# Performance work log

Measured on AMD Instinct MI355X. Metric: run time of the kernel, lower is better.

Reference implementation:

```python
import jax, jax.numpy as jnp
import numpy as np

K = 3  # knnLoss default k


def _knn_loss(source_pc, target_pc, k=K):
    """Faithful translation of knnLoss.forward.

    For each batch: drop exact-zero (0,0,0) points from both clouds
    (emulated via masking for static shapes), find the k nearest *target*
    points for every *source* point (query=source, ref=target), take the
    mean Euclidean distance, then average over batch.
    """

    def per_batch(src, tgt):  # src, tgt: [N, 3]
        src_valid = jnp.any(src != 0.0, axis=-1)  # [Ns] move_zero_point mask
        tgt_valid = jnp.any(tgt != 0.0, axis=-1)  # [Nt]
        s2 = jnp.sum(src * src, axis=-1)          # [Ns]
        t2 = jnp.sum(tgt * tgt, axis=-1)          # [Nt]
        # squared pairwise distances, [Ns, Nt]
        d2 = s2[:, None] + t2[None, :] - 2.0 * (src @ tgt.T)
        d2 = jnp.maximum(d2, 0.0)
        # invalid (zero) target points can never be a neighbor
        d2 = jnp.where(tgt_valid[None, :], d2, jnp.inf)
        neg_top, _ = jax.lax.top_k(-d2, k)        # k smallest squared dists
        dist = jnp.sqrt(-neg_top)                 # [Ns, k] euclidean, like KNN_CUDA
        # mean over valid source points x k neighbors
        num = jnp.sum(jnp.where(src_valid[:, None], dist, 0.0))
        den = jnp.sum(src_valid).astype(dist.dtype) * k
        return num / den

    return jnp.mean(jax.vmap(per_batch)(source_pc, target_pc))


def setup_inputs() -> dict:
    key = jax.random.key(0)
    k1, k2 = jax.random.split(key)
    B, N = 4, 8192
    source_pc = jax.random.normal(k1, (B, N, 3), dtype=jnp.float32)
    target_pc = jax.random.normal(k2, (B, N, 3), dtype=jnp.float32)
    return {"source_pc": source_pc, "target_pc": target_pc}


def reference(source_pc, target_pc):
    return _knn_loss(source_pc, target_pc)
```

## Files before the change

kernel.cpp:

```cpp
#include <hip/hip_runtime.h>
#include <math.h>

#define BATCH 4
#define NPTS 8192
#define TILE 512
#define TSPLIT 16
#define SRC_PER_BLOCK 512
#define SRC_CHUNKS 16
#define NSRC_TOT (BATCH * NPTS)

typedef __attribute__((ext_vector_type(2))) float f2;
typedef __attribute__((ext_vector_type(4))) float f4;

__device__ __forceinline__ f2 pk_fma(f2 a, f2 b, f2 c) {
    f2 d;
    asm("v_pk_fma_f32 %0, %1, %2, %3" : "=v"(d) : "v"(a), "v"(b), "v"(c));
    return d;
}

__device__ __forceinline__ void insert3(float d, float& a0, float& a1, float& a2) {
    float h = fmaxf(a1, d);
    float m = __builtin_amdgcn_fmed3f(a0, a1, d);
    a2 = fminf(a2, h);
    a1 = m;
    a0 = fminf(a0, d);
}

__device__ __forceinline__ void merge33(float a0, float a1, float a2,
                                        float& b0, float& b1, float& b2) {
    float s0 = fminf(a0, b0);
    float h  = fmaxf(a0, b0);
    float m  = fminf(a1, b1);
    float mm = fminf(a2, b2);
    b1 = fminf(h, m);
    b2 = __builtin_amdgcn_fmed3f(h, m, mm);
    b0 = s0;
}

__global__ __launch_bounds__(256) void knn_partial(const float* __restrict__ src,
                                                   const float* __restrict__ tgt,
                                                   float* __restrict__ part,
                                                   float* __restrict__ hdr) {
    __shared__ f4 ts[TILE / 2 * 2];
    const int tid = threadIdx.x;
    const int sc = blockIdx.x, tc = blockIdx.y, b = blockIdx.z;

    if (sc == 0 && tc == 0 && b == 0 && tid < 16) hdr[tid] = 0.0f;

    {
        const float* tb = tgt + ((size_t)b * NPTS + (size_t)tc * TILE + 2 * tid) * 3;
        float x0 = tb[0], y0 = tb[1], z0 = tb[2];
        float x1 = tb[3], y1 = tb[4], z1 = tb[5];
        float w0 = 0.5f * (x0 * x0 + y0 * y0 + z0 * z0);
        float w1 = 0.5f * (x1 * x1 + y1 * y1 + z1 * z1);
        if (!(x0 != 0.f || y0 != 0.f || z0 != 0.f)) w0 = 1.0e38f;
        if (!(x1 != 0.f || y1 != 0.f || z1 != 0.f)) w1 = 1.0e38f;
        ts[2 * tid + 0] = (f4){x0, x1, y0, y1};
        ts[2 * tid + 1] = (f4){z0, z1, w0, w1};
    }
    __syncthreads();

    f2 nx[2], ny[2], nz[2];
    #pragma unroll
    for (int s = 0; s < 2; ++s) {
        int i = sc * SRC_PER_BLOCK + tid + 256 * s;
        const float* sp = src + ((size_t)b * NPTS + i) * 3;
        float ax = sp[0], ay = sp[1], az = sp[2];
        nx[s] = (f2){-ax, -ax};
        ny[s] = (f2){-ay, -ay};
        nz[s] = (f2){-az, -az};
    }

    float c0[2][2], c1[2][2], c2[2][2];
    #pragma unroll
    for (int s = 0; s < 2; ++s)
        for (int h = 0; h < 2; ++h) { c0[s][h] = c1[s][h] = c2[s][h] = 3e38f; }

    #pragma unroll 8
    for (int e = 0; e < TILE / 2; ++e) {
        f4 p = ts[2 * e + 0];
        f4 q = ts[2 * e + 1];
        f2 xs = __builtin_shufflevector(p, p, 0, 1);
        f2 ys = __builtin_shufflevector(p, p, 2, 3);
        f2 zs = __builtin_shufflevector(q, q, 0, 1);
        f2 wh = __builtin_shufflevector(q, q, 2, 3);
        #pragma unroll
        for (int s = 0; s < 2; ++s) {
            f2 v = pk_fma(xs, nx[s], wh);
            v = pk_fma(ys, ny[s], v);
            v = pk_fma(zs, nz[s], v);
            insert3(v.x, c0[s][0], c1[s][0], c2[s][0]);
            insert3(v.y, c0[s][1], c1[s][1], c2[s][1]);
        }
    }

    #pragma unroll
    for (int s = 0; s < 2; ++s) {
        merge33(c0[s][1], c1[s][1], c2[s][1], c0[s][0], c1[s][0], c2[s][0]);
        size_t flat = (size_t)b * NPTS + sc * SRC_PER_BLOCK + tid + 256 * s;
        part[((size_t)tc * 3 + 0) * NSRC_TOT + flat] = c0[s][0];
        part[((size_t)tc * 3 + 1) * NSRC_TOT + flat] = c1[s][0];
        part[((size_t)tc * 3 + 2) * NSRC_TOT + flat] = c2[s][0];
    }
}

__global__ __launch_bounds__(128) void knn_merge(const float* __restrict__ src,
                                                 const float* __restrict__ part,
                                                 float* __restrict__ acc,
                                                 float* __restrict__ cnt,
                                                 unsigned* __restrict__ ticket,
                                                 float* __restrict__ out) {
    const int gid = blockIdx.x * 128 + threadIdx.x;
    const int b = gid >> 13;

    float t0[4], t1[4], t2[4];
    #pragma unroll
    for (int c = 0; c < 4; ++c) { t0[c] = t1[c] = t2[c] = 3e38f; }
    #pragma unroll
    for (int q = 0; q < TSPLIT * 3; ++q)
        insert3(part[(size_t)q * NSRC_TOT + gid], t0[q & 3], t1[q & 3], t2[q & 3]);
    merge33(t0[1], t1[1], t2[1], t0[0], t1[0], t2[0]);
    merge33(t0[3], t1[3], t2[3], t0[2], t1[2], t2[2]);
    merge33(t0[2], t1[2], t2[2], t0[0], t1[0], t2[0]);

    float sx = src[(size_t)gid * 3 + 0];
    float sy = src[(size_t)gid * 3 + 1];
    float sz = src[(size_t)gid * 3 + 2];
    float s2 = sx * sx + sy * sy + sz * sz;
    bool valid = (sx != 0.f) || (sy != 0.f) || (sz != 0.f);
    float d0 = sqrtf(fmaxf(fmaf(2.f, t0[0], s2), 0.f));
    float d1 = sqrtf(fmaxf(fmaf(2.f, t1[0], s2), 0.f));
    float d2 = sqrtf(fmaxf(fmaf(2.f, t2[0], s2), 0.f));
    float s = valid ? (d0 + d1 + d2) : 0.f;
    float c = valid ? 1.f : 0.f;

    for (int off = 32; off >= 1; off >>= 1) {
        s += __shfl_down(s, off);
        c += __shfl_down(c, off);
    }
    __shared__ float red_s[2], red_c[2];
    int wave = threadIdx.x >> 6, lane = threadIdx.x & 63;
    if (lane == 0) { red_s[wave] = s; red_c[wave] = c; }
    __syncthreads();
    if (threadIdx.x == 0) {
        atomicAdd(&acc[b], red_s[0] + red_s[1]);
        atomicAdd(&cnt[b], red_c[0] + red_c[1]);
        __threadfence();
        unsigned t = atomicAdd(ticket, 1u);
        if (t == (unsigned)(gridDim.x - 1)) {
            float loss = 0.f;
            #pragma unroll
            for (int bb = 0; bb < BATCH; ++bb) {
                float as = atomicAdd(&acc[bb], 0.f);
                float ac = atomicAdd(&cnt[bb], 0.f);
                loss += as / (ac * 3.0f);
            }
            out[0] = loss * (1.0f / BATCH);
        }
    }
}

extern "C" void kernel_launch(void* const* d_in, const int* in_sizes, int n_in,
                              void* d_out, int out_size, void* d_ws, size_t ws_size,
                              hipStream_t stream) {
    const float* src = (const float*)d_in[0];
    const float* tgt = (const float*)d_in[1];
    float* out = (float*)d_out;

    float* hdr = (float*)d_ws;
    float* acc = hdr;
    float* cnt = hdr + 4;
    unsigned* ticket = (unsigned*)((char*)d_ws + 32);
    float* part = (float*)((char*)d_ws + 256);

    dim3 g1(SRC_CHUNKS, TSPLIT, BATCH);
    knn_partial<<<g1, 256, 0, stream>>>(src, tgt, part, hdr);

    knn_merge<<<dim3(NSRC_TOT / 128), 128, 0, stream>>>(src, part, acc, cnt, ticket, out);
}
```

Before: 123.0 us.

## Precompute packed target tiles and stream them from global with four sources per thread

Adds a prep kernel that packs the target points and their half-norms, with a sentinel for zero points, into an f4 layout once. The distance kernel now reads these packed targets straight from global memory through a uniform address instead of staging them in LDS behind a barrier. Each thread now handles four source points instead of two, which halves the number of blocks and doubles reuse of each loaded target. The cost is an extra kernel launch, fewer waves available to hide memory latency, and higher register pressure.

```diff
diff --git a/kernel.cpp b/kernel.cpp
--- a/kernel.cpp
+++ b/kernel.cpp
@@ -5,9 +5,11 @@
 #define NPTS 8192
 #define TILE 512
 #define TSPLIT 16
-#define SRC_PER_BLOCK 512
-#define SRC_CHUNKS 16
+#define SRC_PER_THREAD 4
+#define SRC_PER_BLOCK 1024
+#define SRC_CHUNKS 8
 #define NSRC_TOT (BATCH * NPTS)
+#define NGROUP (BATCH * NPTS / 2)
 
 typedef __attribute__((ext_vector_type(2))) float f2;
 typedef __attribute__((ext_vector_type(4))) float f4;
@@ -37,32 +39,32 @@
     b0 = s0;
 }
 
+__global__ __launch_bounds__(256) void knn_prep(const float* __restrict__ tgt,
+                                                f4* __restrict__ tp,
+                                                float* __restrict__ hdr) {
+    int g = blockIdx.x * 256 + threadIdx.x;
+    if (g < 16) hdr[g] = 0.0f;
+    const float* tb = tgt + (size_t)g * 6;
+    float x0 = tb[0], y0 = tb[1], z0 = tb[2];
+    float x1 = tb[3], y1 = tb[4], z1 = tb[5];
+    float w0 = 0.5f * (x0 * x0 + y0 * y0 + z0 * z0);
+    float w1 = 0.5f * (x1 * x1 + y1 * y1 + z1 * z1);
+    if (!(x0 != 0.f || y0 != 0.f || z0 != 0.f)) w0 = 1.0e38f;
+    if (!(x1 != 0.f || y1 != 0.f || z1 != 0.f)) w1 = 1.0e38f;
+    tp[2 * (size_t)g + 0] = (f4){x0, x1, y0, y1};
+    tp[2 * (size_t)g + 1] = (f4){z0, z1, w0, w1};
+}
+
 __global__ __launch_bounds__(256) void knn_partial(const float* __restrict__ src,
-                                                   const float* __restrict__ tgt,
-                                                   float* __restrict__ part,
-                                                   float* __restrict__ hdr) {
-    __shared__ f4 ts[TILE / 2 * 2];
+                                                   const f4* __restrict__ tp,
+                                                   float* __restrict__ part) {
     const int tid = threadIdx.x;
     const int sc = blockIdx.x, tc = blockIdx.y, b = blockIdx.z;
+    int dv = __builtin_amdgcn_mbcnt_lo(0u, 0u);
 
-    if (sc == 0 && tc == 0 && b == 0 && tid < 16) hdr[tid] = 0.0f;
-
-    {
-        const float* tb = tgt + ((size_t)b * NPTS + (size_t)tc * TILE + 2 * tid) * 3;
-        float x0 = tb[0], y0 = tb[1], z0 = tb[2];
-        float x1 = tb[3], y1 = tb[4], z1 = tb[5];
-        float w0 = 0.5f * (x0 * x0 + y0 * y0 + z0 * z0);
-        float w1 = 0.5f * (x1 * x1 + y1 * y1 + z1 * z1);
-        if (!(x0 != 0.f || y0 != 0.f || z0 != 0.f)) w0 = 1.0e38f;
-        if (!(x1 != 0.f || y1 != 0.f || z1 != 0.f)) w1 = 1.0e38f;
-        ts[2 * tid + 0] = (f4){x0, x1, y0, y1};
-        ts[2 * tid + 1] = (f4){z0, z1, w0, w1};
-    }
-    __syncthreads();
-
-    f2 nx[2], ny[2], nz[2];
+    f2 nx[SRC_PER_THREAD], ny[SRC_PER_THREAD], nz[SRC_PER_THREAD];
     #pragma unroll
-    for (int s = 0; s < 2; ++s) {
+    for (int s = 0; s < SRC_PER_THREAD; ++s) {
         int i = sc * SRC_PER_BLOCK + tid + 256 * s;
         const float* sp = src + ((size_t)b * NPTS + i) * 3;
         float ax = sp[0], ay = sp[1], az = sp[2];
@@ -71,21 +73,23 @@
         nz[s] = (f2){-az, -az};
     }
 
-    float c0[2][2], c1[2][2], c2[2][2];
+    float c0[SRC_PER_THREAD][2], c1[SRC_PER_THREAD][2], c2[SRC_PER_THREAD][2];
     #pragma unroll
-    for (int s = 0; s < 2; ++s)
+    for (int s = 0; s < SRC_PER_THREAD; ++s)
         for (int h = 0; h < 2; ++h) { c0[s][h] = c1[s][h] = c2[s][h] = 3e38f; }
+
+    const f4* tbase = tp + ((size_t)b * (NPTS / 2) + (size_t)tc * (TILE / 2)) * 2 + dv;
 
     #pragma unroll 8
     for (int e = 0; e < TILE / 2; ++e) {
-        f4 p = ts[2 * e + 0];
-        f4 q = ts[2 * e + 1];
+        f4 p = tbase[2 * e + 0];
+        f4 q = tbase[2 * e + 1];
         f2 xs = __builtin_shufflevector(p, p, 0, 1);
         f2 ys = __builtin_shufflevector(p, p, 2, 3);
         f2 zs = __builtin_shufflevector(q, q, 0, 1);
         f2 wh = __builtin_shufflevector(q, q, 2, 3);
         #pragma unroll
-        for (int s = 0; s < 2; ++s) {
+        for (int s = 0; s < SRC_PER_THREAD; ++s) {
             f2 v = pk_fma(xs, nx[s], wh);
             v = pk_fma(ys, ny[s], v);
             v = pk_fma(zs, nz[s], v);
@@ -95,7 +99,7 @@
     }
 
     #pragma unroll
-    for (int s = 0; s < 2; ++s) {
+    for (int s = 0; s < SRC_PER_THREAD; ++s) {
         merge33(c0[s][1], c1[s][1], c2[s][1], c0[s][0], c1[s][0], c2[s][0]);
         size_t flat = (size_t)b * NPTS + sc * SRC_PER_BLOCK + tid + 256 * s;
         part[((size_t)tc * 3 + 0) * NSRC_TOT + flat] = c0[s][0];
@@ -171,10 +175,13 @@
     float* acc = hdr;
     float* cnt = hdr + 4;
     unsigned* ticket = (unsigned*)((char*)d_ws + 32);
-    float* part = (float*)((char*)d_ws + 256);
+    f4* tp = (f4*)((char*)d_ws + 256);
+    float* part = (float*)((char*)d_ws + (1u << 20));
+
+    knn_prep<<<dim3(NGROUP / 256), 256, 0, stream>>>(tgt, tp, hdr);
 
     dim3 g1(SRC_CHUNKS, TSPLIT, BATCH);
-    knn_partial<<<g1, 256, 0, stream>>>(src, tgt, part, hdr);
+    knn_partial<<<g1, 256, 0, stream>>>(src, tp, part);
 
     knn_merge<<<dim3(NSRC_TOT / 128), 128, 0, stream>>>(src, part, acc, cnt, ticket, out);
 }
```

Measured after the change: 159.1 us. 29.3% more time.

## Template KNN kernels on target split and prefetch LDS tile entries

Applied to the files above, without the earlier changes.

Turns the partial and merge kernels into templates on the target split count and tile size. When the workspace is large enough it uses 32 target splits of 256 points, doubling the grid to raise occupancy at the cost of more partial-result traffic and a heavier merge. It also software-prefetches the next shared-memory entry inside the inner loop, adds an occupancy hint to launch bounds, and widens the merge kernel to 256 threads with 8 independent top-3 accumulators. The partial buffer is moved to a 1 MiB offset in the workspace.

```diff
diff --git a/kernel.cpp b/kernel.cpp
--- a/kernel.cpp
+++ b/kernel.cpp
@@ -3,10 +3,6 @@
 
 #define BATCH 4
 #define NPTS 8192
-#define TILE 512
-#define TSPLIT 16
-#define SRC_PER_BLOCK 512
-#define SRC_CHUNKS 16
 #define NSRC_TOT (BATCH * NPTS)
 
 typedef __attribute__((ext_vector_type(2))) float f2;
@@ -37,33 +33,35 @@
     b0 = s0;
 }
 
-__global__ __launch_bounds__(256) void knn_partial(const float* __restrict__ src,
-                                                   const float* __restrict__ tgt,
-                                                   float* __restrict__ part,
-                                                   float* __restrict__ hdr) {
-    __shared__ f4 ts[TILE / 2 * 2];
+template <int TSPLITT, int TILET>
+__global__ __launch_bounds__(256, 6)
+void knn_partial(const float* __restrict__ src, const float* __restrict__ tgt,
+                 float* __restrict__ part, float* __restrict__ hdr) {
+    constexpr int ENTRIES = TILET / 2;
+    __shared__ f4 ts[ENTRIES * 2];
     const int tid = threadIdx.x;
     const int sc = blockIdx.x, tc = blockIdx.y, b = blockIdx.z;
 
     if (sc == 0 && tc == 0 && b == 0 && tid < 16) hdr[tid] = 0.0f;
 
-    {
-        const float* tb = tgt + ((size_t)b * NPTS + (size_t)tc * TILE + 2 * tid) * 3;
+    for (int e = tid; e < ENTRIES; e += 256) {
+        const float* tb = tgt + ((size_t)b * NPTS + (size_t)tc * TILET + 2 * e) * 3;
         float x0 = tb[0], y0 = tb[1], z0 = tb[2];
         float x1 = tb[3], y1 = tb[4], z1 = tb[5];
         float w0 = 0.5f * (x0 * x0 + y0 * y0 + z0 * z0);
         float w1 = 0.5f * (x1 * x1 + y1 * y1 + z1 * z1);
         if (!(x0 != 0.f || y0 != 0.f || z0 != 0.f)) w0 = 1.0e38f;
         if (!(x1 != 0.f || y1 != 0.f || z1 != 0.f)) w1 = 1.0e38f;
-        ts[2 * tid + 0] = (f4){x0, x1, y0, y1};
-        ts[2 * tid + 1] = (f4){z0, z1, w0, w1};
+        ts[2 * e + 0] = (f4){x0, x1, y0, y1};
+        ts[2 * e + 1] = (f4){z0, z1, w0, w1};
     }
     __syncthreads();
 
+    const int src_per_block = 512;
     f2 nx[2], ny[2], nz[2];
     #pragma unroll
     for (int s = 0; s < 2; ++s) {
-        int i = sc * SRC_PER_BLOCK + tid + 256 * s;
+        int i = sc * src_per_block + tid + 256 * s;
         const float* sp = src + ((size_t)b * NPTS + i) * 3;
         float ax = sp[0], ay = sp[1], az = sp[2];
         nx[s] = (f2){-ax, -ax};
@@ -76,10 +74,14 @@
     for (int s = 0; s < 2; ++s)
         for (int h = 0; h < 2; ++h) { c0[s][h] = c1[s][h] = c2[s][h] = 3e38f; }
 
-    #pragma unroll 8
-    for (int e = 0; e < TILE / 2; ++e) {
-        f4 p = ts[2 * e + 0];
-        f4 q = ts[2 * e + 1];
+    f4 p = ts[0], q = ts[1];
+    #pragma unroll 4
+    for (int e = 0; e < ENTRIES; ++e) {
+        f4 pn, qn;
+        if (e + 1 < ENTRIES) {
+            pn = ts[2 * e + 2];
+            qn = ts[2 * e + 3];
+        }
         f2 xs = __builtin_shufflevector(p, p, 0, 1);
         f2 ys = __builtin_shufflevector(p, p, 2, 3);
         f2 zs = __builtin_shufflevector(q, q, 0, 1);
@@ -92,36 +94,41 @@
             insert3(v.x, c0[s][0], c1[s][0], c2[s][0]);
             insert3(v.y, c0[s][1], c1[s][1], c2[s][1]);
         }
+        p = pn;
+        q = qn;
     }
 
     #pragma unroll
     for (int s = 0; s < 2; ++s) {
         merge33(c0[s][1], c1[s][1], c2[s][1], c0[s][0], c1[s][0], c2[s][0]);
-        size_t flat = (size_t)b * NPTS + sc * SRC_PER_BLOCK + tid + 256 * s;
+        size_t flat = (size_t)b * NPTS + sc * src_per_block + tid + 256 * s;
         part[((size_t)tc * 3 + 0) * NSRC_TOT + flat] = c0[s][0];
         part[((size_t)tc * 3 + 1) * NSRC_TOT + flat] = c1[s][0];
         part[((size_t)tc * 3 + 2) * NSRC_TOT + flat] = c2[s][0];
     }
 }
 
-__global__ __launch_bounds__(128) void knn_merge(const float* __restrict__ src,
-                                                 const float* __restrict__ part,
-                                                 float* __restrict__ acc,
-                                                 float* __restrict__ cnt,
-                                                 unsigned* __restrict__ ticket,
-                                                 float* __restrict__ out) {
-    const int gid = blockIdx.x * 128 + threadIdx.x;
+template <int TSPLITT>
+__global__ __launch_bounds__(256)
+void knn_merge(const float* __restrict__ src, const float* __restrict__ part,
+               float* __restrict__ acc, float* __restrict__ cnt,
+               unsigned* __restrict__ ticket, float* __restrict__ out) {
+    const int gid = blockIdx.x * 256 + threadIdx.x;
     const int b = gid >> 13;
 
-    float t0[4], t1[4], t2[4];
+    float t0[8], t1[8], t2[8];
     #pragma unroll
-    for (int c = 0; c < 4; ++c) { t0[c] = t1[c] = t2[c] = 3e38f; }
+    for (int c = 0; c < 8; ++c) { t0[c] = t1[c] = t2[c] = 3e38f; }
     #pragma unroll
-    for (int q = 0; q < TSPLIT * 3; ++q)
-        insert3(part[(size_t)q * NSRC_TOT + gid], t0[q & 3], t1[q & 3], t2[q & 3]);
+    for (int q = 0; q < TSPLITT * 3; ++q)
+        insert3(part[(size_t)q * NSRC_TOT + gid], t0[q & 7], t1[q & 7], t2[q & 7]);
     merge33(t0[1], t1[1], t2[1], t0[0], t1[0], t2[0]);
     merge33(t0[3], t1[3], t2[3], t0[2], t1[2], t2[2]);
+    merge33(t0[5], t1[5], t2[5], t0[4], t1[4], t2[4]);
+    merge33(t0[7], t1[7], t2[7], t0[6], t1[6], t2[6]);
     merge33(t0[2], t1[2], t2[2], t0[0], t1[0], t2[0]);
+    merge33(t0[6], t1[6], t2[6], t0[4], t1[4], t2[4]);
+    merge33(t0[4], t1[4], t2[4], t0[0], t1[0], t2[0]);
 
     float sx = src[(size_t)gid * 3 + 0];
     float sy = src[(size_t)gid * 3 + 1];
@@ -138,13 +145,13 @@
         s += __shfl_down(s, off);
         c += __shfl_down(c, off);
     }
-    __shared__ float red_s[2], red_c[2];
+    __shared__ float red_s[4], red_c[4];
     int wave = threadIdx.x >> 6, lane = threadIdx.x & 63;
     if (lane == 0) { red_s[wave] = s; red_c[wave] = c; }
     __syncthreads();
     if (threadIdx.x == 0) {
-        atomicAdd(&acc[b], red_s[0] + red_s[1]);
-        atomicAdd(&cnt[b], red_c[0] + red_c[1]);
+        atomicAdd(&acc[b], red_s[0] + red_s[1] + red_s[2] + red_s[3]);
+        atomicAdd(&cnt[b], red_c[0] + red_c[1] + red_c[2] + red_c[3]);
         __threadfence();
         unsigned t = atomicAdd(ticket, 1u);
         if (t == (unsigned)(gridDim.x - 1)) {
@@ -171,10 +178,17 @@
     float* acc = hdr;
     float* cnt = hdr + 4;
     unsigned* ticket = (unsigned*)((char*)d_ws + 32);
-    float* part = (float*)((char*)d_ws + 256);
+    float* part = (float*)((char*)d_ws + (1u << 20));
 
-    dim3 g1(SRC_CHUNKS, TSPLIT, BATCH);
-    knn_partial<<<g1, 256, 0, stream>>>(src, tgt, part, hdr);
-
-    knn_merge<<<dim3(NSRC_TOT / 128), 128, 0, stream>>>(src, part, acc, cnt, ticket, out);
+    if (ws_size >= (size_t)(14u << 20)) {
+        dim3 g1(16, 32, BATCH);
+        knn_partial<32, 256><<<g1, 256, 0, stream>>>(src, tgt, part, hdr);
+        knn_merge<32><<<dim3(NSRC_TOT / 256), 256, 0, stream>>>(src, part, acc, cnt,
+                                                                ticket, out);
+    } else {
+        dim3 g1(16, 16, BATCH);
+        knn_partial<16, 512><<<g1, 256, 0, stream>>>(src, tgt, part, hdr);
+        knn_merge<16><<<dim3(NSRC_TOT / 256), 256, 0, stream>>>(src, part, acc, cnt,
+                                                                ticket, out);
+    }
 }
```

Result: no change. 122.0 us (-0.9%).
